# Performance work log

Hardware: AMD Instinct MI355X
Metric: run time of the kernel (lower is better)

The kernel has to match this reference:

```python
import jax, jax.numpy as jnp
import numpy as np

B, L, M, N, C = 2, 1024, 8, 16, 16
H, W, D = 64, 64, 16  # d == c: one histogram plane per feature channel


def setup_inputs() -> dict:
    key = jax.random.key(0)
    k1, k2, k3, k4, k5 = jax.random.split(key, 5)
    feats_src_dst = jax.random.normal(k1, (B, L, N, C), dtype=jnp.float32)
    voxels_src = jax.random.randint(k2, (B, L, 2), 0, 64).astype(jnp.int32)
    voxels_dst = jax.random.randint(k3, (B, L, 2), 0, 64).astype(jnp.int32)
    idxs_src = jax.random.randint(k4, (B, L, M), 0, L).astype(jnp.int32)
    idxs_dst = jax.random.randint(k5, (B, L, N), 0, L).astype(jnp.int32)
    return {
        "feats_src_dst": feats_src_dst,
        "voxels_src": voxels_src,
        "voxels_dst": voxels_dst,
        "idxs_src": idxs_src,
        "idxs_dst": idxs_dst,
    }


def reference(feats_src_dst, voxels_src, voxels_dst, idxs_src, idxs_dst):
    b, l, m = idxs_src.shape
    n = idxs_dst.shape[-1]
    c = feats_src_dst.shape[-1]
    dt = feats_src_dst.dtype

    gather = jax.vmap(lambda arr, idx: arr[idx])  # per-batch fancy gather

    s = idxs_src                                   # [b,l,m]  src KNN of each anchor
    dd = gather(idxs_dst, s)                       # [b,l,m,n] dst KNN of each src neighbor
    vsrc = gather(voxels_src.astype(dt), s)        # [b,l,m,2]
    vdst = gather(voxels_dst.astype(dt), dd)       # [b,l,m,n,2]
    wf = gather(feats_src_dst, s)                  # [b,l,m,n,c] vote weights

    # translation -> centered histogram bin
    t = vdst - vsrc[:, :, :, None, :]              # [b,l,m,n,2] (y,x)
    by = jnp.floor(t[..., 0]).astype(jnp.int32) + H // 2
    bx = jnp.floor(t[..., 1]).astype(jnp.int32) + W // 2
    valid = (by >= 0) & (by < H) & (bx >= 0) & (bx < W)
    by = jnp.clip(by, 0, H - 1)
    bx = jnp.clip(bx, 0, W - 1)
    wf = jnp.where(valid[..., None], wf, jnp.zeros((), dt))

    bi = jnp.broadcast_to(jnp.arange(b)[:, None, None, None], (b, l, m, n))
    li = jnp.broadcast_to(jnp.arange(l)[None, :, None, None], (b, l, m, n))

    hist = jnp.zeros((b, l, H, W, c), dt)
    hist = hist.at[bi, li, by, bx].add(wf)         # scatter-add voting
    return jnp.transpose(hist, (0, 1, 4, 2, 3))    # [b,l,c,h,w]
```

## Files before the change

### kernel.cpp

```cpp
#include <hip/hip_runtime.h>

#define B_ 2
#define L_ 1024
#define M_ 8
#define N_ 16
#define C_ 16
#define H_ 64
#define W_ 64

#define NVOTE (M_ * N_)
#define WPAD  (C_ + 1)
#define PLANE (H_ * W_)

__global__ __launch_bounds__(256) void hough_vote_kernel(
    const float* __restrict__ feats,
    const int*   __restrict__ voxels_src,
    const int*   __restrict__ voxels_dst,
    const int*   __restrict__ idxs_src,
    const int*   __restrict__ idxs_dst,
    float*       __restrict__ out)
{
    const int bl  = blockIdx.x;
    const int b   = bl >> 10;
    const int tid = threadIdx.x;

    __shared__ int   s_src[M_];
    __shared__ int   s_bin[NVOTE];
    __shared__ float s_w[NVOTE * WPAD];
    __shared__ float s_plane[PLANE];

    if (tid < M_) s_src[tid] = idxs_src[bl * M_ + tid];
    __syncthreads();

    #pragma unroll
    for (int i = 0; i < (NVOTE * C_) / 256; ++i) {
        int idx  = i * 256 + tid;
        int m    = idx >> 8;
        int off  = idx & 255;
        int s    = s_src[m];
        float v  = feats[((size_t)(b * L_ + s)) * (N_ * C_) + off];
        int vote = (m << 4) | (off >> 4);
        int c    = off & 15;
        s_w[vote * WPAD + c] = v;
    }

    if (tid < NVOTE) {
        int m  = tid >> 4;
        int n  = tid & 15;
        int s  = s_src[m];
        int vy = voxels_src[(b * L_ + s) * 2 + 0];
        int vx = voxels_src[(b * L_ + s) * 2 + 1];
        int dd = idxs_dst[(b * L_ + s) * N_ + n];
        int dy = voxels_dst[(b * L_ + dd) * 2 + 0];
        int dx = voxels_dst[(b * L_ + dd) * 2 + 1];
        int by = dy - vy + H_ / 2;
        int bx = dx - vx + W_ / 2;
        bool valid = (by >= 0) & (by < H_) & (bx >= 0) & (bx < W_);
        s_bin[tid] = valid ? (by * W_ + bx) : -1;
    }
    __syncthreads();

    float*  outb = out + (size_t)bl * (C_ * PLANE);
    float4* p4   = (float4*)s_plane;

    for (int c = 0; c < C_; ++c) {
        #pragma unroll
        for (int i = 0; i < PLANE / 4 / 256; ++i)
            p4[i * 256 + tid] = make_float4(0.f, 0.f, 0.f, 0.f);
        __syncthreads();

        if (tid < NVOTE) {
            int bin = s_bin[tid];
            if (bin >= 0) atomicAdd(&s_plane[bin], s_w[tid * WPAD + c]);
        }
        __syncthreads();

        float4* o4 = (float4*)(outb + c * PLANE);
        #pragma unroll
        for (int i = 0; i < PLANE / 4 / 256; ++i)
            o4[i * 256 + tid] = p4[i * 256 + tid];
        __syncthreads();
    }
}

extern "C" void kernel_launch(void* const* d_in, const int* in_sizes, int n_in,
                              void* d_out, int out_size, void* d_ws, size_t ws_size,
                              hipStream_t stream) {
    const float* feats      = (const float*)d_in[0];
    const int*   voxels_src = (const int*)d_in[1];
    const int*   voxels_dst = (const int*)d_in[2];
    const int*   idxs_src   = (const int*)d_in[3];
    const int*   idxs_dst   = (const int*)d_in[4];
    float*       out        = (float*)d_out;

    hough_vote_kernel<<<B_ * L_, 256, 0, stream>>>(
        feats, voxels_src, voxels_dst, idxs_src, idxs_dst, out);
}
```

Measured before the change: 530.5 us.

## Split histogram work into one block per (anchor, channel) plane

Launches one block per output channel plane instead of one block per anchor that loops over all sixteen channels. Each block recomputes the vote bins and loads only its own channel's weight, so the per-channel barrier loop goes away and there are sixteen times as many blocks to spread across CUs. In exchange the index and voxel gathers are repeated once per channel, and feature loads become strided by channel. The kernel stays bound by the 268MB of output writes.

```diff
diff --git a/kernel.cpp b/kernel.cpp
--- a/kernel.cpp
+++ b/kernel.cpp
@@ -9,10 +9,9 @@
 #define W_ 64
 
 #define NVOTE (M_ * N_)
-#define WPAD  (C_ + 1)
 #define PLANE (H_ * W_)
 
-__global__ __launch_bounds__(256) void hough_vote_kernel(
+__global__ __launch_bounds__(256) void hough_vote_plane_kernel(
     const float* __restrict__ feats,
     const int*   __restrict__ voxels_src,
     const int*   __restrict__ voxels_dst,
@@ -20,67 +19,45 @@
     const int*   __restrict__ idxs_dst,
     float*       __restrict__ out)
 {
-    const int bl  = blockIdx.x;
+    const int gb  = blockIdx.x;
+    const int bl  = gb >> 4;
+    const int c   = gb & (C_ - 1);
     const int b   = bl >> 10;
     const int tid = threadIdx.x;
 
-    __shared__ int   s_src[M_];
-    __shared__ int   s_bin[NVOTE];
-    __shared__ float s_w[NVOTE * WPAD];
     __shared__ float s_plane[PLANE];
 
-    if (tid < M_) s_src[tid] = idxs_src[bl * M_ + tid];
+    float w   = 0.f;
+    int   bin = -1;
+    if (tid < NVOTE) {
+        int m    = tid >> 4;
+        int n    = tid & (N_ - 1);
+        int s    = idxs_src[bl * M_ + m];
+        int base = b * L_ + s;
+        int2 vs  = ((const int2*)voxels_src)[base];
+        int  dd  = idxs_dst[base * N_ + n];
+        int2 vd  = ((const int2*)voxels_dst)[b * L_ + dd];
+        int by = vd.x - vs.x + H_ / 2;
+        int bx = vd.y - vs.y + W_ / 2;
+        if (by >= 0 && by < H_ && bx >= 0 && bx < W_) {
+            bin = by * W_ + bx;
+            w   = feats[((size_t)base * N_ + n) * C_ + c];
+        }
+    }
+
+    float4* p4 = (float4*)s_plane;
+    #pragma unroll
+    for (int i = 0; i < PLANE / 4 / 256; ++i)
+        p4[i * 256 + tid] = make_float4(0.f, 0.f, 0.f, 0.f);
     __syncthreads();
 
-    #pragma unroll
-    for (int i = 0; i < (NVOTE * C_) / 256; ++i) {
-        int idx  = i * 256 + tid;
-        int m    = idx >> 8;
-        int off  = idx & 255;
-        int s    = s_src[m];
-        float v  = feats[((size_t)(b * L_ + s)) * (N_ * C_) + off];
-        int vote = (m << 4) | (off >> 4);
-        int c    = off & 15;
-        s_w[vote * WPAD + c] = v;
-    }
-
-    if (tid < NVOTE) {
-        int m  = tid >> 4;
-        int n  = tid & 15;
-        int s  = s_src[m];
-        int vy = voxels_src[(b * L_ + s) * 2 + 0];
-        int vx = voxels_src[(b * L_ + s) * 2 + 1];
-        int dd = idxs_dst[(b * L_ + s) * N_ + n];
-        int dy = voxels_dst[(b * L_ + dd) * 2 + 0];
-        int dx = voxels_dst[(b * L_ + dd) * 2 + 1];
-        int by = dy - vy + H_ / 2;
-        int bx = dx - vx + W_ / 2;
-        bool valid = (by >= 0) & (by < H_) & (bx >= 0) & (bx < W_);
-        s_bin[tid] = valid ? (by * W_ + bx) : -1;
-    }
+    if (bin >= 0) atomicAdd(&s_plane[bin], w);
     __syncthreads();
 
-    float*  outb = out + (size_t)bl * (C_ * PLANE);
-    float4* p4   = (float4*)s_plane;
-
-    for (int c = 0; c < C_; ++c) {
-        #pragma unroll
-        for (int i = 0; i < PLANE / 4 / 256; ++i)
-            p4[i * 256 + tid] = make_float4(0.f, 0.f, 0.f, 0.f);
-        __syncthreads();
-
-        if (tid < NVOTE) {
-            int bin = s_bin[tid];
-            if (bin >= 0) atomicAdd(&s_plane[bin], s_w[tid * WPAD + c]);
-        }
-        __syncthreads();
-
-        float4* o4 = (float4*)(outb + c * PLANE);
-        #pragma unroll
-        for (int i = 0; i < PLANE / 4 / 256; ++i)
-            o4[i * 256 + tid] = p4[i * 256 + tid];
-        __syncthreads();
-    }
+    float4* o4 = (float4*)(out + ((size_t)bl * C_ + c) * PLANE);
+    #pragma unroll
+    for (int i = 0; i < PLANE / 4 / 256; ++i)
+        o4[i * 256 + tid] = p4[i * 256 + tid];
 }
 
 extern "C" void kernel_launch(void* const* d_in, const int* in_sizes, int n_in,
@@ -93,6 +70,6 @@
     const int*   idxs_dst   = (const int*)d_in[4];
     float*       out        = (float*)d_out;
 
-    hough_vote_kernel<<<B_ * L_, 256, 0, stream>>>(
+    hough_vote_plane_kernel<<<B_ * L_ * C_, 256, 0, stream>>>(
         feats, voxels_src, voxels_dst, idxs_src, idxs_dst, out);
 }
```

New measurement: 527.2 us. Within noise of the previous version (-0.6%).
